# Optimization experiments

Measured on AMD Instinct MI355X. Metric: run time of the kernel, lower is better.

The kernel has to match this reference:

```python
import jax, jax.numpy as jnp
import numpy as np

W = 128      # windowed_attn_w
H = 8        # num_heads
D = 1024     # model_dim
DK = D // 2  # dim_key = dim_value


def setup_inputs() -> dict:
    key = jax.random.key(0)
    ks = jax.random.split(key, 10)
    B, S = 8, 4096
    qk = jax.random.normal(ks[0], (B, D, S), dtype=jnp.float32)
    v = jax.random.normal(ks[1], (B, D, S), dtype=jnp.float32)
    masks = jnp.ones((B, 1, S), dtype=jnp.float32)
    sc = 1.0 / np.sqrt(D)
    Wq = jax.random.normal(ks[2], (DK, D), dtype=jnp.float32) * sc
    bq = jnp.zeros((DK,), dtype=jnp.float32)
    Wk = jax.random.normal(ks[3], (DK, D), dtype=jnp.float32) * sc
    bk = jnp.zeros((DK,), dtype=jnp.float32)
    Wv = jax.random.normal(ks[4], (DK, D), dtype=jnp.float32) * sc
    bv = jnp.zeros((DK,), dtype=jnp.float32)
    Wo = jax.random.normal(ks[5], (D, DK), dtype=jnp.float32) * (1.0 / np.sqrt(DK))
    bo = jnp.zeros((D,), dtype=jnp.float32)
    return dict(qk=qk, v=v, masks=masks, Wq=Wq, bq=bq, Wk=Wk, bk=bk,
                Wv=Wv, bv=bv, Wo=Wo, bo=bo)


def _to_patches(x):
    # [b, d, s] -> [(b*num_patches), d, W]  (non-overlapping windows)
    b, d, s = x.shape
    np_ = s // W
    return x.reshape(b, d, np_, W).transpose(0, 2, 1, 3).reshape(b * np_, d, W)


def reference(qk, v, masks, Wq, bq, Wk, bk, Wv, bv, Wo, bo):
    B, _, S = qk.shape
    np_ = S // W
    qp = _to_patches(qk)          # [BN, D, W]  (query == key input)
    vp = _to_patches(v)           # [BN, D, W]
    mp = _to_patches(masks)       # [BN, 1, W]  key mask per window

    # 1x1 conv1d projections == channel matmuls
    q = jnp.einsum('ed,bdw->bew', Wq, qp) + bq[:, None]   # [BN, DK, W]
    k = jnp.einsum('ed,bdw->bew', Wk, qp) + bk[:, None]
    val = jnp.einsum('ed,bdw->bew', Wv, vp) + bv[:, None]

    BN = q.shape[0]
    dh = DK // H
    qh = q.reshape(BN, H, dh, W)
    kh = k.reshape(BN, H, dh, W)
    vh = val.reshape(BN, H, dh, W)

    scores = jnp.einsum('bhdi,bhdj->bhij', qh, kh) / jnp.sqrt(jnp.asarray(dh, qh.dtype))
    # mask keys (j axis): [BN,1,W] -> [BN,1,1,W]
    scores = jnp.where(mp[:, :, None, :] > 0, scores, jnp.asarray(-1e9, scores.dtype))
    attn = jax.nn.softmax(scores, axis=-1)
    o = jnp.einsum('bhij,bhdj->bhdi', attn, vh).reshape(BN, DK, W)

    # out_proj: GELU (exact) then 1x1 conv1d DK -> D
    o = jax.nn.gelu(o, approximate=False)
    out = jnp.einsum('de,bew->bdw', Wo, o) + bo[:, None]   # [BN, D, W]

    # undo reshape -> [B, D, S]
    out = out.reshape(B, np_, D, W).transpose(0, 2, 1, 3).reshape(B, D, S)
    out = out * masks
    return out
```

## Files before the change

kernel.cpp:

```cpp
#include <hip/hip_runtime.h>

typedef unsigned short u16b;
typedef __attribute__((ext_vector_type(8))) short short8;
typedef __attribute__((ext_vector_type(4))) float float4v;

#define DEV __device__ __forceinline__

DEV float b2f(u16b u){ union{unsigned int i; float f;} x; x.i=((unsigned int)u)<<16; return x.f; }
DEV u16b f2b(float f){ union{float f; unsigned int i;} x; x.f=f;
  return (u16b)((x.i + 0x7fffu + ((x.i>>16)&1u))>>16); }

DEV short8 ld8(const void* base, size_t idx, int f){
  if (f) return *(const short8*)((const u16b*)base + idx);
  const float* p = (const float*)base + idx;
  float4v a = *(const float4v*)p;
  float4v b = *(const float4v*)(p+4);
  short8 r;
  r[0]=(short)f2b(a[0]); r[1]=(short)f2b(a[1]); r[2]=(short)f2b(a[2]); r[3]=(short)f2b(a[3]);
  r[4]=(short)f2b(b[0]); r[5]=(short)f2b(b[1]); r[6]=(short)f2b(b[2]); r[7]=(short)f2b(b[3]);
  return r;
}

__global__ void sniff_k(const void* __restrict__ qk, int* __restrict__ flag){
  const u16b* u = (const u16b*)qk;
  int t = threadIdx.x;
  u16b x = u[(size_t)2*t*257];
  int e = (x>>7)&0xFF;
  int ok = (e>=100 && e<=134 && (x&0x7FFF)!=0) ? 1 : 0;
  unsigned long long b = __ballot(ok);
  __shared__ int cnt[4];
  if ((t&63)==0) cnt[t>>6] = __popcll(b);
  __syncthreads();
  if (t==0) *flag = (cnt[0]+cnt[1]+cnt[2]+cnt[3] >= 128) ? 1 : 0;
}

struct IngestArgs {
  const void* src[9];
  int n[9];
  int off[9];
};

__global__ __launch_bounds__(256)
void ingest_k(IngestArgs a, u16b* __restrict__ dst, const int* __restrict__ flag){
  const int f = *flag;
  const int stride = gridDim.x*blockDim.x;
#pragma unroll
  for (int t=0;t<9;t++){
    const void* s = a.src[t];
    int n = a.n[t], o = a.off[t];
    for (int i = blockIdx.x*blockDim.x + threadIdx.x; i < n; i += stride){
      float v = f ? b2f(((const u16b*)s)[i]) : ((const float*)s)[i];
      dst[o + i] = f2b(v);
    }
  }
}

__global__ __launch_bounds__(256,4)
void transpose_k(const void* __restrict__ in, u16b* __restrict__ out,
                 const int* __restrict__ flag, int R, int C)
{
  __shared__ u16b tile[64][72];
  const int f = *flag;
  const int c0 = blockIdx.x*64;
  const int r0 = blockIdx.y*64;
  const size_t base = (size_t)blockIdx.z * (size_t)R * (size_t)C;
  const int tid = threadIdx.x;
#pragma unroll
  for (int i=0;i<2;i++){
    int idx = i*256+tid;
    int rr = idx>>3;
    int cc = (idx&7)*8;
    *(short8*)&tile[rr][cc] = ld8(in, base + (size_t)(r0+rr)*C + c0 + cc, f);
  }
  __syncthreads();
#pragma unroll
  for (int i=0;i<2;i++){
    int idx = i*256+tid;
    int cc = idx>>3;
    int rr = (idx&7)*8;
    short8 v;
#pragma unroll
    for (int j=0;j<8;j++) v[j] = (short)tile[rr+j][cc];
    *(short8*)&out[base + (size_t)(c0+cc)*R + r0 + rr] = v;
  }
}

template<int MODE>
__global__ __launch_bounds__(256,2)
void gemm_kt(const u16b* __restrict__ A, const u16b* __restrict__ B,
             void* __restrict__ Cv, const u16b* __restrict__ bias,
             const u16b* __restrict__ mask, const int* __restrict__ flag,
             int M, int N, int K)
{
  __shared__ u16b a_sh[128][40];
  __shared__ u16b b_sh[128][40];
  const int f = (MODE==2) ? *flag : 0;
  const int tid  = threadIdx.x;
  const int lane = tid & 63;
  const int wv   = tid >> 6;
  const int wm   = (wv>>1)*64, wn = (wv&1)*64;
  const int q    = lane>>4, ln = lane&15;
  const int m0   = blockIdx.y*128, n0 = blockIdx.x*128;

  float4v acc[4][4];
#pragma unroll
  for (int i=0;i<4;i++)
#pragma unroll
    for (int j=0;j<4;j++) acc[i][j] = float4v{0.f,0.f,0.f,0.f};

  for (int k0=0; k0<K; k0+=32){
    __syncthreads();
#pragma unroll
    for (int i=0;i<2;i++){
      int idx=i*256+tid, row=idx>>2, ch=(idx&3)*8;
      *(short8*)&a_sh[row][ch] = *(const short8*)&A[(size_t)(m0+row)*K + k0 + ch];
      *(short8*)&b_sh[row][ch] = *(const short8*)&B[(size_t)(n0+row)*K + k0 + ch];
    }
    __syncthreads();
    short8 af[4], bfr[4];
#pragma unroll
    for (int mt=0;mt<4;mt++) af[mt]  = *(const short8*)&a_sh[wm+mt*16+ln][q*8];
#pragma unroll
    for (int nt=0;nt<4;nt++) bfr[nt] = *(const short8*)&b_sh[wn+nt*16+ln][q*8];
#pragma unroll
    for (int mt=0;mt<4;mt++)
#pragma unroll
      for (int nt=0;nt<4;nt++)
        acc[mt][nt] = __builtin_amdgcn_mfma_f32_16x16x32_bf16(
            af[mt], bfr[nt], acc[mt][nt], 0,0,0);
  }

#pragma unroll
  for (int mt=0;mt<4;mt++)
#pragma unroll
    for (int nt=0;nt<4;nt++)
#pragma unroll
      for (int r=0;r<4;r++){
        int gm = m0 + wm + mt*16 + q*4 + r;
        int gn = n0 + wn + nt*16 + ln;
        float v = acc[mt][nt][r];
        if (MODE==0) v += b2f(bias[gn]);
        else         v += b2f(bias[gm]);
        if (MODE==2){
          v *= b2f(mask[gn]);
          size_t oidx = ((size_t)(gn>>12)*1024 + gm)*4096 + (gn&4095);
          if (f) ((u16b*)Cv)[oidx] = f2b(v);
          else   ((float*)Cv)[oidx] = v;
        } else {
          ((u16b*)Cv)[(size_t)gm*N + gn] = f2b(v);
        }
      }
}

__global__ __launch_bounds__(256,2)
void attn_k(const u16b* __restrict__ QT, const u16b* __restrict__ KT,
            const u16b* __restrict__ V2, const u16b* __restrict__ mask,
            u16b* __restrict__ GT)
{
  __shared__ u16b v_sh[64][136];
  __shared__ u16b p_sh[4][32][136];
  const int bid = blockIdx.x;
  const int w = bid>>3, h = bid&7;
  const int tid = threadIdx.x, lane = tid&63, wv = tid>>6;
  const int q = lane>>4, ln = lane&15;
  const size_t cb = (size_t)w*128;

#pragma unroll
  for (int i=0;i<4;i++){
    int idx=i*256+tid, row=idx>>4, ch=(idx&15)*8;
    *(short8*)&v_sh[row][ch] =
        *(const short8*)&V2[(size_t)(h*64+row)*32768 + cb + ch];
  }

  short8 qf[2][2], kf[8][2];
#pragma unroll
  for (int mt=0;mt<2;mt++)
#pragma unroll
    for (int ks=0;ks<2;ks++)
      qf[mt][ks] = *(const short8*)&QT[(cb + wv*32 + mt*16 + ln)*512 + h*64 + ks*32 + q*8];
#pragma unroll
  for (int nt=0;nt<8;nt++)
#pragma unroll
    for (int ks=0;ks<2;ks++)
      kf[nt][ks] = *(const short8*)&KT[(cb + nt*16 + ln)*512 + h*64 + ks*32 + q*8];

  float4v sa[2][8];
#pragma unroll
  for (int mt=0;mt<2;mt++)
#pragma unroll
    for (int nt=0;nt<8;nt++) sa[mt][nt] = float4v{0.f,0.f,0.f,0.f};
#pragma unroll
  for (int ks=0;ks<2;ks++)
#pragma unroll
    for (int mt=0;mt<2;mt++)
#pragma unroll
      for (int nt=0;nt<8;nt++)
        sa[mt][nt] = __builtin_amdgcn_mfma_f32_16x16x32_bf16(
            qf[mt][ks], kf[nt][ks], sa[mt][nt], 0,0,0);

  float mk[8];
#pragma unroll
  for (int nt=0;nt<8;nt++) mk[nt] = b2f(mask[cb + nt*16 + ln]);
#pragma unroll
  for (int mt=0;mt<2;mt++)
#pragma unroll
    for (int nt=0;nt<8;nt++)
#pragma unroll
      for (int r=0;r<4;r++){
        float s = sa[mt][nt][r]*0.125f;
        sa[mt][nt][r] = (mk[nt] > 0.0f) ? s : -1e9f;
      }

  float mrow[2][4], lrow[2][4];
#pragma unroll
  for (int mt=0;mt<2;mt++)
#pragma unroll
    for (int r=0;r<4;r++){
      float m = -3e38f;
#pragma unroll
      for (int nt=0;nt<8;nt++) m = fmaxf(m, sa[mt][nt][r]);
#pragma unroll
      for (int d=1; d<16; d<<=1) m = fmaxf(m, __shfl_xor(m, d));
      mrow[mt][r] = m;
    }
#pragma unroll
  for (int mt=0;mt<2;mt++)
#pragma unroll
    for (int nt=0;nt<8;nt++)
#pragma unroll
      for (int r=0;r<4;r++)
        sa[mt][nt][r] = __expf(sa[mt][nt][r] - mrow[mt][r]);
#pragma unroll
  for (int mt=0;mt<2;mt++)
#pragma unroll
    for (int r=0;r<4;r++){
      float l = 0.f;
#pragma unroll
      for (int nt=0;nt<8;nt++) l += sa[mt][nt][r];
#pragma unroll
      for (int d=1; d<16; d<<=1) l += __shfl_xor(l, d);
      lrow[mt][r] = l;
    }

#pragma unroll
  for (int mt=0;mt<2;mt++)
#pragma unroll
    for (int nt=0;nt<8;nt++)
#pragma unroll
      for (int r=0;r<4;r++)
        p_sh[wv][mt*16 + q*4 + r][nt*16 + ln] = f2b(sa[mt][nt][r]);
  __syncthreads();

  float4v oa[2][4];
#pragma unroll
  for (int mt=0;mt<2;mt++)
#pragma unroll
    for (int nt=0;nt<4;nt++) oa[mt][nt] = float4v{0.f,0.f,0.f,0.f};
#pragma unroll
  for (int ks=0;ks<4;ks++){
    short8 pf[2], vf[4];
#pragma unroll
    for (int mt=0;mt<2;mt++) pf[mt] = *(const short8*)&p_sh[wv][mt*16+ln][ks*32+q*8];
#pragma unroll
    for (int nt=0;nt<4;nt++) vf[nt] = *(const short8*)&v_sh[nt*16+ln][ks*32+q*8];
#pragma unroll
    for (int mt=0;mt<2;mt++)
#pragma unroll
      for (int nt=0;nt<4;nt++)
        oa[mt][nt] = __builtin_amdgcn_mfma_f32_16x16x32_bf16(
            pf[mt], vf[nt], oa[mt][nt], 0,0,0);
  }

#pragma unroll
  for (int mt=0;mt<2;mt++)
#pragma unroll
    for (int nt=0;nt<4;nt++)
#pragma unroll
      for (int r=0;r<4;r++){
        float x = oa[mt][nt][r] * (1.0f / lrow[mt][r]);
        float g = 0.5f * x * (1.0f + erff(x * 0.70710678118f));
        GT[(cb + wv*32 + mt*16 + q*4 + r)*512 + h*64 + nt*16 + ln] = f2b(g);
      }
}

extern "C" void kernel_launch(void* const* d_in, const int* in_sizes, int n_in,
                              void* d_out, int out_size, void* d_ws, size_t ws_size,
                              hipStream_t stream)
{
  const void* qk    = d_in[0];
  const void* v     = d_in[1];
  const void* masks = d_in[2];

  char* ws = (char*)d_ws;
  int*  flag  = (int*)ws;
  u16b* wbase = (u16b*)(ws + 1024);
  const int OWQ=0, OWK=524288, OWV=1048576, OWO=1572864;
  const int OBQ=2097152, OBK=2097664, OBV=2098176, OBO=2098688, OMSK=2099712;

  u16b* Xt = (u16b*)d_out;
  u16b* QT = (u16b*)(ws + ((size_t) 8<<20));
  u16b* KT = (u16b*)(ws + ((size_t)40<<20));
  u16b* V2 = (u16b*)(ws + ((size_t)72<<20));
  u16b* GT = KT;

  sniff_k<<<1,256,0,stream>>>(qk, flag);

  IngestArgs ia;
  ia.src[0]=d_in[3]; ia.n[0]=524288; ia.off[0]=OWQ;
  ia.src[1]=d_in[5]; ia.n[1]=524288; ia.off[1]=OWK;
  ia.src[2]=d_in[7]; ia.n[2]=524288; ia.off[2]=OWV;
  ia.src[3]=d_in[9]; ia.n[3]=524288; ia.off[3]=OWO;
  ia.src[4]=d_in[4]; ia.n[4]=512;    ia.off[4]=OBQ;
  ia.src[5]=d_in[6]; ia.n[5]=512;    ia.off[5]=OBK;
  ia.src[6]=d_in[8]; ia.n[6]=512;    ia.off[6]=OBV;
  ia.src[7]=d_in[10];ia.n[7]=1024;   ia.off[7]=OBO;
  ia.src[8]=masks;   ia.n[8]=32768;  ia.off[8]=OMSK;
  ingest_k<<<1024,256,0,stream>>>(ia, wbase, flag);

  dim3 tg(64,16,8);
  transpose_k<<<tg,256,0,stream>>>(qk, Xt, flag, 1024, 4096);
  gemm_kt<0><<<dim3(4,256),256,0,stream>>>(Xt, wbase+OWQ, QT, wbase+OBQ, nullptr, flag, 32768, 512, 1024);
  gemm_kt<0><<<dim3(4,256),256,0,stream>>>(Xt, wbase+OWK, KT, wbase+OBK, nullptr, flag, 32768, 512, 1024);
  transpose_k<<<tg,256,0,stream>>>(v, Xt, flag, 1024, 4096);
  gemm_kt<1><<<dim3(256,4),256,0,stream>>>(wbase+OWV, Xt, V2, wbase+OBV, nullptr, flag, 512, 32768, 1024);
  attn_k<<<2048,256,0,stream>>>(QT, KT, V2, wbase+OMSK, GT);
  gemm_kt<2><<<dim3(256,8),256,0,stream>>>(wbase+OWO, GT, d_out, wbase+OBO, wbase+OMSK, flag, 1024, 32768, 512);
}
```

Baseline: 600.9 us.

## Use direct global-to-LDS loads with swizzle, fuse Q/K GEMMs and transposes

The GEMM tile staging now uses global_load_lds (16-byte direct-to-LDS loads) into an XOR-swizzled shared layout instead of going through registers, which cuts VGPR traffic and LDS bank conflicts. The Q and K projections become one GEMM with N=1024 whose epilogue splits the output into the QT and KT buffers. Both input transposes run as one launch writing separate workspace buffers. This relies on Wq and Wk sitting next to each other in the weight buffer, uses more workspace, and adds a full vmcnt wait per k-step with no double buffering.

```diff
diff --git a/kernel.cpp b/kernel.cpp
--- a/kernel.cpp
+++ b/kernel.cpp
@@ -9,6 +9,12 @@
 DEV float b2f(u16b u){ union{unsigned int i; float f;} x; x.i=((unsigned int)u)<<16; return x.f; }
 DEV u16b f2b(float f){ union{float f; unsigned int i;} x; x.f=f;
   return (u16b)((x.i + 0x7fffu + ((x.i>>16)&1u))>>16); }
+
+DEV void g2l16(const u16b* g, u16b* l){
+  __builtin_amdgcn_global_load_lds(
+      (const __attribute__((address_space(1))) void*)g,
+      (__attribute__((address_space(3))) void*)l, 16, 0, 0);
+}
 
 DEV short8 ld8(const void* base, size_t idx, int f){
   if (f) return *(const short8*)((const u16b*)base + idx);
@@ -56,14 +62,20 @@
 }
 
 __global__ __launch_bounds__(256,4)
-void transpose_k(const void* __restrict__ in, u16b* __restrict__ out,
-                 const int* __restrict__ flag, int R, int C)
+void transpose2_k(const void* __restrict__ qk, const void* __restrict__ vv,
+                  u16b* __restrict__ outq, u16b* __restrict__ outv,
+                  const int* __restrict__ flag)
 {
   __shared__ u16b tile[64][72];
   const int f = *flag;
+  const int R = 1024, C = 4096;
+  const int z = blockIdx.z;
+  const void* in = (z<8) ? qk : vv;
+  u16b* out = (z<8) ? outq : outv;
+  const int zz = z&7;
   const int c0 = blockIdx.x*64;
   const int r0 = blockIdx.y*64;
-  const size_t base = (size_t)blockIdx.z * (size_t)R * (size_t)C;
+  const size_t base = (size_t)zz * (size_t)R * (size_t)C;
   const int tid = threadIdx.x;
 #pragma unroll
   for (int i=0;i<2;i++){
@@ -92,8 +104,8 @@
              const u16b* __restrict__ mask, const int* __restrict__ flag,
              int M, int N, int K)
 {
-  __shared__ u16b a_sh[128][40];
-  __shared__ u16b b_sh[128][40];
+  __shared__ __align__(16) u16b a_sh[4096];
+  __shared__ __align__(16) u16b b_sh[4096];
   const int f = (MODE==2) ? *flag : 0;
   const int tid  = threadIdx.x;
   const int lane = tid & 63;
@@ -102,6 +114,21 @@
   const int q    = lane>>4, ln = lane&15;
   const int m0   = blockIdx.y*128, n0 = blockIdx.x*128;
 
+  const int L0 = wv*64 + lane;
+  const int r0s = L0>>2;
+  const int kc0 = (L0&3) ^ ((r0s>>1)&3);
+  const int L1 = (wv+4)*64 + lane;
+  const int r1s = L1>>2;
+  const int kc1 = (L1&3) ^ ((r1s>>1)&3);
+  const size_t ga0 = (size_t)(m0+r0s)*K + (kc0<<3);
+  const size_t ga1 = (size_t)(m0+r1s)*K + (kc1<<3);
+  const size_t gb0 = (size_t)(n0+r0s)*K + (kc0<<3);
+  const size_t gb1 = (size_t)(n0+r1s)*K + (kc1<<3);
+
+  const int sw  = (q ^ ((ln>>1)&3))<<3;
+  const int aoff = (wm+ln)*32 + sw;
+  const int boff = (wn+ln)*32 + sw;
+
   float4v acc[4][4];
 #pragma unroll
   for (int i=0;i<4;i++)
@@ -110,18 +137,17 @@
 
   for (int k0=0; k0<K; k0+=32){
     __syncthreads();
-#pragma unroll
-    for (int i=0;i<2;i++){
-      int idx=i*256+tid, row=idx>>2, ch=(idx&3)*8;
-      *(short8*)&a_sh[row][ch] = *(const short8*)&A[(size_t)(m0+row)*K + k0 + ch];
-      *(short8*)&b_sh[row][ch] = *(const short8*)&B[(size_t)(n0+row)*K + k0 + ch];
-    }
+    g2l16(&A[ga0 + k0], &a_sh[wv*512]);
+    g2l16(&A[ga1 + k0], &a_sh[(wv+4)*512]);
+    g2l16(&B[gb0 + k0], &b_sh[wv*512]);
+    g2l16(&B[gb1 + k0], &b_sh[(wv+4)*512]);
+    asm volatile("s_waitcnt vmcnt(0)" ::: "memory");
     __syncthreads();
     short8 af[4], bfr[4];
 #pragma unroll
-    for (int mt=0;mt<4;mt++) af[mt]  = *(const short8*)&a_sh[wm+mt*16+ln][q*8];
-#pragma unroll
-    for (int nt=0;nt<4;nt++) bfr[nt] = *(const short8*)&b_sh[wn+nt*16+ln][q*8];
+    for (int mt=0;mt<4;mt++) af[mt]  = *(const short8*)&a_sh[aoff + mt*512];
+#pragma unroll
+    for (int nt=0;nt<4;nt++) bfr[nt] = *(const short8*)&b_sh[boff + nt*512];
 #pragma unroll
     for (int mt=0;mt<4;mt++)
 #pragma unroll
@@ -139,13 +165,16 @@
         int gm = m0 + wm + mt*16 + q*4 + r;
         int gn = n0 + wn + nt*16 + ln;
         float v = acc[mt][nt][r];
-        if (MODE==0) v += b2f(bias[gn]);
+        if (MODE==3) v += b2f(bias[gn]);
         else         v += b2f(bias[gm]);
         if (MODE==2){
           v *= b2f(mask[gn]);
           size_t oidx = ((size_t)(gn>>12)*1024 + gm)*4096 + (gn&4095);
           if (f) ((u16b*)Cv)[oidx] = f2b(v);
           else   ((float*)Cv)[oidx] = v;
+        } else if (MODE==3){
+          u16b* dst = (u16b*)Cv + ((size_t)(gn>>9)<<24);
+          dst[(size_t)gm*512 + (gn&511)] = f2b(v);
         } else {
           ((u16b*)Cv)[(size_t)gm*N + gn] = f2b(v);
         }
@@ -297,11 +326,12 @@
   const int OWQ=0, OWK=524288, OWV=1048576, OWO=1572864;
   const int OBQ=2097152, OBK=2097664, OBV=2098176, OBO=2098688, OMSK=2099712;
 
-  u16b* Xt = (u16b*)d_out;
-  u16b* QT = (u16b*)(ws + ((size_t) 8<<20));
-  u16b* KT = (u16b*)(ws + ((size_t)40<<20));
-  u16b* V2 = (u16b*)(ws + ((size_t)72<<20));
-  u16b* GT = KT;
+  u16b* QT  = (u16b*)(ws + ((size_t)  8<<20));
+  u16b* KT  = (u16b*)(ws + ((size_t) 40<<20));
+  u16b* V2  = (u16b*)(ws + ((size_t) 72<<20));
+  u16b* Xtq = (u16b*)(ws + ((size_t)104<<20));
+  u16b* Xtv = (u16b*)(ws + ((size_t)168<<20));
+  u16b* GT  = KT;
 
   sniff_k<<<1,256,0,stream>>>(qk, flag);
 
@@ -317,12 +347,9 @@
   ia.src[8]=masks;   ia.n[8]=32768;  ia.off[8]=OMSK;
   ingest_k<<<1024,256,0,stream>>>(ia, wbase, flag);
 
-  dim3 tg(64,16,8);
-  transpose_k<<<tg,256,0,stream>>>(qk, Xt, flag, 1024, 4096);
-  gemm_kt<0><<<dim3(4,256),256,0,stream>>>(Xt, wbase+OWQ, QT, wbase+OBQ, nullptr, flag, 32768, 512, 1024);
-  gemm_kt<0><<<dim3(4,256),256,0,stream>>>(Xt, wbase+OWK, KT, wbase+OBK, nullptr, flag, 32768, 512, 1024);
-  transpose_k<<<tg,256,0,stream>>>(v, Xt, flag, 1024, 4096);
-  gemm_kt<1><<<dim3(256,4),256,0,stream>>>(wbase+OWV, Xt, V2, wbase+OBV, nullptr, flag, 512, 32768, 1024);
+  transpose2_k<<<dim3(64,16,16),256,0,stream>>>(qk, v, Xtq, Xtv, flag);
+  gemm_kt<3><<<dim3(8,256),256,0,stream>>>(Xtq, wbase+OWQ, QT, wbase+OBQ, nullptr, flag, 32768, 1024, 1024);
+  gemm_kt<1><<<dim3(256,4),256,0,stream>>>(wbase+OWV, Xtv, V2, wbase+OBV, nullptr, flag, 512, 32768, 1024);
   attn_k<<<2048,256,0,stream>>>(QT, KT, V2, wbase+OMSK, GT);
   gemm_kt<2><<<dim3(256,8),256,0,stream>>>(wbase+OWO, GT, d_out, wbase+OBO, wbase+OMSK, flag, 1024, 32768, 512);
 }
```

Measured after the change: 591.2 us. No clear change (-1.6%).
